# Kernel optimization log

Hardware: AMD Instinct MI355X
Metric: run time of the kernel (lower is better)

Reference implementation:

```python
import jax, jax.numpy as jnp
import numpy as np

N_NODES = 100000
N_EDGES = 100000
NNZ = 3200000
D_IN, D_HID, N_CLS = 512, 16, 7
NEG_SLOPE = 0.2


def _segment_softmax(scores, seg, num_segments, sorted_seg):
    m = jax.ops.segment_max(scores, seg, num_segments=num_segments,
                            indices_are_sorted=sorted_seg)
    ex = jnp.exp(scores - m[seg])
    s = jax.ops.segment_sum(ex, seg, num_segments=num_segments,
                            indices_are_sorted=sorted_seg)
    return ex / (s[seg] + 1e-9)


def _hypergat_layer(X, W, a1, a2, node_idx, edge_idx):
    # X: [N, din] -> h: [N, dout]
    h = X @ W
    hv = h[node_idx]                                   # [nnz, dout] gather
    # phase 1: node -> hyperedge attention (softmax within each hyperedge)
    s1 = jax.nn.leaky_relu(hv @ a1, NEG_SLOPE)         # [nnz]
    alpha = _segment_softmax(s1, edge_idx, N_EDGES, True)
    e = jax.ops.segment_sum(alpha[:, None] * hv, edge_idx,
                            num_segments=N_EDGES, indices_are_sorted=True)
    # phase 2: hyperedge -> node attention (softmax over edges incident to node)
    ev = e[edge_idx]                                   # [nnz, dout] gather
    s2 = jax.nn.leaky_relu(jnp.concatenate([hv, ev], axis=-1) @ a2, NEG_SLOPE)
    beta = _segment_softmax(s2, node_idx, N_NODES, False)
    out = jax.ops.segment_sum(beta[:, None] * ev, node_idx,
                              num_segments=N_NODES)
    return out


def setup_inputs() -> dict:
    key = jax.random.key(0)
    ks = jax.random.split(key, 8)
    H = jax.random.normal(ks[0], (N_NODES, D_IN), dtype=jnp.float32)
    node_idx = jax.random.randint(ks[1], (NNZ,), 0, N_NODES)
    edge_idx = jnp.sort(jax.random.randint(ks[2], (NNZ,), 0, N_EDGES))
    g1 = 1.0 / np.sqrt(D_IN)
    g2 = 1.0 / np.sqrt(D_HID)
    W1 = jax.random.uniform(ks[3], (D_IN, D_HID), jnp.float32, -g1, g1)
    a1_1 = jax.random.uniform(ks[4], (D_HID,), jnp.float32, -g2, g2)
    a2_1 = jax.random.uniform(ks[5], (2 * D_HID,), jnp.float32, -g2, g2)
    W2 = jax.random.uniform(ks[6], (D_HID, N_CLS), jnp.float32, -g2, g2)
    k7, k8 = jax.random.split(ks[7])
    gc = 1.0 / np.sqrt(N_CLS)
    a1_2 = jax.random.uniform(k7, (N_CLS,), jnp.float32, -gc, gc)
    a2_2 = jax.random.uniform(k8, (2 * N_CLS,), jnp.float32, -gc, gc)
    return {"H": H, "W1": W1, "a1_1": a1_1, "a2_1": a2_1,
            "W2": W2, "a1_2": a1_2, "a2_2": a2_2,
            "node_idx": node_idx, "edge_idx": edge_idx}


def reference(H, W1, a1_1, a2_1, W2, a1_2, a2_2, node_idx, edge_idx):
    H1 = _hypergat_layer(H, W1, a1_1, a2_1, node_idx, edge_idx)   # [N, 16]
    X2 = jax.nn.elu(H1)                                           # dropout off (eval)
    H2 = _hypergat_layer(X2, W2, a1_2, a2_2, node_idx, edge_idx)  # [N, 7]
    logp = jax.nn.log_softmax(H2, axis=1)
    return (logp, H1, H2)
```

## Files before the change

kernel.cpp:

```cpp
#include <hip/hip_runtime.h>
#include <hip/hip_bf16.h>
#include <math.h>

#define N_NODES 100000
#define N_EDGESC 100000
#define NNZ_C   3200000
#define D_IN    512
#define D_HID   16
#define N_CLS   7
#define NBK     782

#define G_GEMM 1563
#define G_EOFF 12500
#define G_HIST 250
#define G_BIN  250

typedef short short8 __attribute__((ext_vector_type(8)));
typedef float f32x4  __attribute__((ext_vector_type(4)));

__device__ __forceinline__ unsigned short f2bf_rn(float x) {
  unsigned int u = __float_as_uint(x);
  u += 0x7fff + ((u >> 16) & 1);
  return (unsigned short)(u >> 16);
}
__device__ __forceinline__ float bf2f(unsigned short b) {
  return __uint_as_float(((unsigned int)b) << 16);
}

__device__ __forceinline__ void eoff_body(int b, const int* __restrict__ eidx,
                                          int* __restrict__ eoff) {
  int i = b * 256 + threadIdx.x;
  if (i >= NNZ_C) return;
  int ec = eidx[i];
  int ep = (i == 0) ? -1 : eidx[i - 1];
  for (int e = ep + 1; e <= ec; ++e) eoff[e] = i;
  if (i == NNZ_C - 1) {
    for (int e = ec + 1; e <= N_EDGESC; ++e) eoff[e] = NNZ_C;
  }
}

__device__ __forceinline__ void hist_body(int b, const int* __restrict__ nidx,
                                          int* __restrict__ gcnt) {
  __shared__ int lh[NBK];
  int t = threadIdx.x;
  for (int i = t; i < NBK; i += 256) lh[i] = 0;
  __syncthreads();
  int base = b * 12800;
  for (int it = 0; it < 50; ++it) {
    int i = base + it * 256 + t;
    if (i < NNZ_C) atomicAdd(&lh[nidx[i] >> 7], 1);
  }
  __syncthreads();
  for (int i = t; i < NBK; i += 256) {
    int c = lh[i];
    if (c) atomicAdd(&gcnt[i], c);
  }
}

__device__ __forceinline__ void bin_body(int b, const int* __restrict__ nidx,
                                         const int* __restrict__ eidx,
                                         int* __restrict__ bcur, int* __restrict__ binned) {
  __shared__ int lh[NBK];
  __shared__ int gb[NBK];
  int t = threadIdx.x;
  for (int i = t; i < NBK; i += 256) lh[i] = 0;
  __syncthreads();
  int base = b * 12800;
  for (int it = 0; it < 50; ++it) {
    int i = base + it * 256 + t;
    if (i < NNZ_C) atomicAdd(&lh[nidx[i] >> 7], 1);
  }
  __syncthreads();
  for (int i = t; i < NBK; i += 256) {
    int c = lh[i];
    gb[i] = c ? atomicAdd(&bcur[i], c) : 0;
    lh[i] = 0;
  }
  __syncthreads();
  for (int it = 0; it < 50; ++it) {
    int i = base + it * 256 + t;
    if (i < NNZ_C) {
      int v = nidx[i], e = eidx[i];
      int bk = v >> 7;
      int r = atomicAdd(&lh[bk], 1);
      binned[gb[bk] + r] = e | ((v & 127) << 20);
    }
  }
}

__global__ void bscan_kernel(const int* __restrict__ gcnt, int* __restrict__ boff,
                             int* __restrict__ bcur) {
  __shared__ int lds[1024];
  int t = threadIdx.x;
  int v = (t < NBK) ? gcnt[t] : 0;
  lds[t] = v;
  __syncthreads();
  for (int d = 1; d < 1024; d <<= 1) {
    int u = (t >= d) ? lds[t - d] : 0;
    __syncthreads();
    lds[t] += u;
    __syncthreads();
  }
  if (t < NBK) {
    boff[t + 1] = lds[t];
    bcur[t] = lds[t] - v;
  }
  if (t == 0) boff[0] = 0;
}

__global__ void csr_kernel(const int* __restrict__ binned, const int* __restrict__ boff,
                           int* __restrict__ noff, int* __restrict__ perm_e, int N) {
  __shared__ int lh[128];
  __shared__ int lsc[128];
  __shared__ int lcur[128];
  int b = blockIdx.x;
  int t = threadIdx.x;
  int s = boff[b], e = boff[b + 1];
  if (t < 128) lh[t] = 0;
  __syncthreads();
  for (int i = s + t; i < e; i += 256) {
    atomicAdd(&lh[binned[i] >> 20], 1);
  }
  __syncthreads();
  if (t < 128) lsc[t] = lh[t];
  __syncthreads();
  for (int d = 1; d < 128; d <<= 1) {
    int u = (t < 128 && t >= d) ? lsc[t - d] : 0;
    __syncthreads();
    if (t < 128) lsc[t] += u;
    __syncthreads();
  }
  if (t < 128) {
    int excl = lsc[t] - lh[t];
    lcur[t] = excl;
    int n = b * 128 + t;
    if (n <= N) noff[n] = s + excl;
  }
  __syncthreads();
  for (int i = s + t; i < e; i += 256) {
    int p = binned[i];
    int r = atomicAdd(&lcur[p >> 20], 1);
    perm_e[s + r] = p & 0xFFFFF;
  }
}

__device__ __forceinline__ void gemm1_body(int b,
    const float* __restrict__ X, const float* __restrict__ W,
    const float* __restrict__ a1, const float* __restrict__ a2,
    float* __restrict__ Hout, float2* __restrict__ phv) {
  int wid = b * 4 + (threadIdx.x >> 6);
  if (wid >= 6250) return;
  int lane = threadIdx.x & 63;
  int col  = lane & 15;
  int quad = lane >> 4;

  short8 wh[16], wl[16];
#pragma unroll
  for (int c = 0; c < 16; ++c) {
#pragma unroll
    for (int j = 0; j < 8; ++j) {
      float w = W[(c * 32 + quad * 8 + j) * 16 + col];
      unsigned short h = f2bf_rn(w);
      wh[c][j] = (short)h;
      wl[c][j] = (short)f2bf_rn(w - bf2f(h));
    }
  }

  int rowbase = wid * 16;
  const float4* Xr = (const float4*)(X + (size_t)(rowbase + col) * D_IN) + quad * 2;

  f32x4 acc_hh = {0.f, 0.f, 0.f, 0.f};
  f32x4 acc_hl = {0.f, 0.f, 0.f, 0.f};
  f32x4 acc_lh = {0.f, 0.f, 0.f, 0.f};

  float4 u0 = Xr[0], u1 = Xr[1];
#pragma unroll
  for (int c = 0; c < 16; ++c) {
    float4 n0, n1;
    if (c < 15) { n0 = Xr[(c + 1) * 8]; n1 = Xr[(c + 1) * 8 + 1]; }
    float xs[8] = {u0.x, u0.y, u0.z, u0.w, u1.x, u1.y, u1.z, u1.w};
    short8 ah, al;
#pragma unroll
    for (int j = 0; j < 8; ++j) {
      unsigned short h = f2bf_rn(xs[j]);
      ah[j] = (short)h;
      al[j] = (short)f2bf_rn(xs[j] - bf2f(h));
    }
    acc_hh = __builtin_amdgcn_mfma_f32_16x16x32_bf16(ah, wh[c], acc_hh, 0, 0, 0);
    acc_hl = __builtin_amdgcn_mfma_f32_16x16x32_bf16(ah, wl[c], acc_hl, 0, 0, 0);
    acc_lh = __builtin_amdgcn_mfma_f32_16x16x32_bf16(al, wh[c], acc_lh, 0, 0, 0);
    u0 = n0; u1 = n1;
  }

  float a1c = a1[col], a2c = a2[col];
#pragma unroll
  for (int r = 0; r < 4; ++r) {
    float v = acc_hh[r] + acc_hl[r] + acc_lh[r];
    int row = rowbase + quad * 4 + r;
    Hout[(size_t)row * 16 + col] = v;
    float p1 = v * a1c, p2 = v * a2c;
#pragma unroll
    for (int d = 1; d < 16; d <<= 1) { p1 += __shfl_xor(p1, d); p2 += __shfl_xor(p2, d); }
    if (col == 0) phv[row] = make_float2(p1, p2);
  }
}

__global__ __launch_bounds__(256) void k1_kernel(
    const float* __restrict__ X, const float* __restrict__ W1,
    const float* __restrict__ a1, const float* __restrict__ a2,
    float* __restrict__ Hout, float2* __restrict__ phv,
    const int* __restrict__ eidx, int* __restrict__ eoff,
    const int* __restrict__ nidx, int* __restrict__ gcnt) {
  int b = blockIdx.x;
  if (b < G_GEMM) {
    gemm1_body(b, X, W1, a1, a2, Hout, phv);
  } else if (b < G_GEMM + G_EOFF) {
    eoff_body(b - G_GEMM, eidx, eoff);
  } else {
    hist_body(b - G_GEMM - G_EOFF, nidx, gcnt);
  }
}

template <int D, int GROUP>
__device__ __forceinline__ void edge_body(
    const float* __restrict__ h, const float2* __restrict__ phv,
    const float* __restrict__ a2, const int* __restrict__ eoff,
    const int* __restrict__ nidx, float* __restrict__ eout,
    float* __restrict__ pe, int E, int wave, int lane) {
  constexpr int NG = 64 / GROUP;
  if (wave >= E) return;
  int o0 = eoff[wave], o1 = eoff[wave + 1];
  int g = lane / GROUP, t = lane % GROUP;
  if (o0 == o1) {
    if (g == 0) {
      if (t < D) eout[(size_t)wave * D + t] = 0.f;
      if (t == 0) pe[wave] = 0.f;
    }
    return;
  }
  float m = -1e30f, l = 0.f, acc = 0.f;
  for (int i = o0 + g; i < o1; i += 2 * NG) {
    int i2 = i + NG;
    bool okb = i2 < o1;
    int va = nidx[i];
    int vb = okb ? nidx[i2] : va;
    float pa_ = phv[va].x;
    float pb_ = phv[vb].x;
    float ha = (t < D) ? h[(size_t)va * D + t] : 0.f;
    float hb = (t < D) ? h[(size_t)vb * D + t] : 0.f;
    float sa = pa_ > 0.f ? pa_ : 0.2f * pa_;
    float sb = pb_ > 0.f ? pb_ : 0.2f * pb_;
    if (!okb) sb = -1e30f;
    float mn = fmaxf(m, fmaxf(sa, sb));
    float eo = __expf(m - mn);
    float exa = __expf(sa - mn);
    float exb = __expf(sb - mn);
    l = l * eo + exa + exb;
    acc = acc * eo + exa * ha + exb * hb;
    m = mn;
  }
#pragma unroll
  for (int d = GROUP; d < 64; d <<= 1) {
    float mo = __shfl_xor(m, d), lo = __shfl_xor(l, d), ao = __shfl_xor(acc, d);
    float mn = fmaxf(m, mo);
    float e0 = __expf(m - mn), e1x = __expf(mo - mn);
    l = l * e0 + lo * e1x;
    acc = acc * e0 + ao * e1x;
    m = mn;
  }
  float val = acc / (l + 1e-9f);
  float pav = (t < D) ? val * a2[D + t] : 0.f;
#pragma unroll
  for (int d = 1; d < GROUP; d <<= 1) pav += __shfl_xor(pav, d);
  if (g == 0) {
    if (t < D) eout[(size_t)wave * D + t] = val;
    if (t == 0) pe[wave] = pav;
  }
}

template <int D, int GROUP>
__global__ void edge_kernel(const float* __restrict__ h, const float2* __restrict__ phv,
                            const float* __restrict__ a2, const int* __restrict__ eoff,
                            const int* __restrict__ nidx, float* __restrict__ eout,
                            float* __restrict__ pe, int E) {
  int wave = (blockIdx.x * blockDim.x + threadIdx.x) >> 6;
  edge_body<D, GROUP>(h, phv, a2, eoff, nidx, eout, pe, E, wave, threadIdx.x & 63);
}

__global__ void k3_kernel(const int* __restrict__ nidx, const int* __restrict__ eidx,
                          int* __restrict__ bcur, int* __restrict__ binned,
                          const float* __restrict__ h1g, const float2* __restrict__ phv,
                          const float* __restrict__ a2_1, const int* __restrict__ eoff,
                          float* __restrict__ e1, float* __restrict__ pe) {
  int b = blockIdx.x;
  if (b < G_BIN) {
    bin_body(b, nidx, eidx, bcur, binned);
  } else {
    int wave = (b - G_BIN) * 4 + (threadIdx.x >> 6);
    edge_body<D_HID, 16>(h1g, phv, a2_1, eoff, nidx, e1, pe, N_EDGESC,
                         wave, threadIdx.x & 63);
  }
}

__global__ void node1_kernel(float2* phv, const float* __restrict__ e1,
                             const float* __restrict__ pe, const int* __restrict__ noff,
                             const int* __restrict__ perm_e, float* __restrict__ H1out,
                             float* __restrict__ h2g, const float* __restrict__ W2,
                             const float* __restrict__ a1_2, const float* __restrict__ a2_2,
                             int N) {
  int wave = (blockIdx.x * blockDim.x + threadIdx.x) >> 6;
  int lane = threadIdx.x & 63;
  if (wave >= N) return;
  int o0 = noff[wave], o1 = noff[wave + 1];
  int g = lane >> 4, t = lane & 15;
  float ph = phv[wave].y;
  float m = -1e30f, l = 0.f, acc = 0.f;
  for (int i = o0 + g; i < o1; i += 8) {
    int i2 = i + 4;
    bool okb = i2 < o1;
    int ea = perm_e[i];
    int eb = okb ? perm_e[i2] : ea;
    float pa_ = ph + pe[ea];
    float pb_ = ph + pe[eb];
    float va = e1[(size_t)ea * 16 + t];
    float vb = e1[(size_t)eb * 16 + t];
    float sa = pa_ > 0.f ? pa_ : 0.2f * pa_;
    float sb = pb_ > 0.f ? pb_ : 0.2f * pb_;
    if (!okb) sb = -1e30f;
    float mn = fmaxf(m, fmaxf(sa, sb));
    float eo = __expf(m - mn);
    float exa = __expf(sa - mn);
    float exb = __expf(sb - mn);
    l = l * eo + exa + exb;
    acc = acc * eo + exa * va + exb * vb;
    m = mn;
  }
#pragma unroll
  for (int d = 16; d < 64; d <<= 1) {
    float mo = __shfl_xor(m, d), lo = __shfl_xor(l, d), ao = __shfl_xor(acc, d);
    float mn = fmaxf(m, mo);
    float e0 = __expf(m - mn), e1x = __expf(mo - mn);
    l = l * e0 + lo * e1x;
    acc = acc * e0 + ao * e1x;
    m = mn;
  }
  float val = acc / (l + 1e-9f);
  if (g == 0) H1out[(size_t)wave * 16 + t] = val;
  float x = val > 0.f ? val : expm1f(val);
  float p1 = 0.f, p2 = 0.f, myh2 = 0.f;
#pragma unroll
  for (int j = 0; j < N_CLS; ++j) {
    float term = x * W2[t * N_CLS + j];
#pragma unroll
    for (int d = 1; d < 16; d <<= 1) term += __shfl_xor(term, d);
    p1 += term * a1_2[j];
    p2 += term * a2_2[j];
    if (t == j) myh2 = term;
  }
  if (g == 0) {
    if (t < N_CLS) h2g[(size_t)wave * N_CLS + t] = myh2;
    if (t == 0) phv[wave] = make_float2(p1, p2);
  }
}

__global__ void node2_kernel(const float2* __restrict__ phv, const float* __restrict__ e2,
                             const float* __restrict__ pe, const int* __restrict__ noff,
                             const int* __restrict__ perm_e, float* __restrict__ H2out,
                             float* __restrict__ logp, int N) {
  int wave = (blockIdx.x * blockDim.x + threadIdx.x) >> 6;
  int lane = threadIdx.x & 63;
  if (wave >= N) return;
  int o0 = noff[wave], o1 = noff[wave + 1];
  int g = lane >> 3, t = lane & 7;
  float ph = phv[wave].y;
  float m = -1e30f, l = 0.f, acc = 0.f;
  for (int i = o0 + g; i < o1; i += 16) {
    int i2 = i + 8;
    bool okb = i2 < o1;
    int ea = perm_e[i];
    int eb = okb ? perm_e[i2] : ea;
    float pa_ = ph + pe[ea];
    float pb_ = ph + pe[eb];
    float va = (t < N_CLS) ? e2[(size_t)ea * N_CLS + t] : 0.f;
    float vb = (t < N_CLS) ? e2[(size_t)eb * N_CLS + t] : 0.f;
    float sa = pa_ > 0.f ? pa_ : 0.2f * pa_;
    float sb = pb_ > 0.f ? pb_ : 0.2f * pb_;
    if (!okb) sb = -1e30f;
    float mn = fmaxf(m, fmaxf(sa, sb));
    float eo = __expf(m - mn);
    float exa = __expf(sa - mn);
    float exb = __expf(sb - mn);
    l = l * eo + exa + exb;
    acc = acc * eo + exa * va + exb * vb;
    m = mn;
  }
#pragma unroll
  for (int d = 8; d < 64; d <<= 1) {
    float mo = __shfl_xor(m, d), lo = __shfl_xor(l, d), ao = __shfl_xor(acc, d);
    float mn = fmaxf(m, mo);
    float e0 = __expf(m - mn), e1x = __expf(mo - mn);
    l = l * e0 + lo * e1x;
    acc = acc * e0 + ao * e1x;
    m = mn;
  }
  float val = acc / (l + 1e-9f);
  if (g == 0 && t < N_CLS) H2out[(size_t)wave * N_CLS + t] = val;
  float xm = (t < N_CLS) ? val : -1e30f;
#pragma unroll
  for (int d = 1; d < 8; d <<= 1) xm = fmaxf(xm, __shfl_xor(xm, d));
  float se = (t < N_CLS) ? __expf(val - xm) : 0.f;
#pragma unroll
  for (int d = 1; d < 8; d <<= 1) se += __shfl_xor(se, d);
  float lg = logf(se);
  if (g == 0 && t < N_CLS) logp[(size_t)wave * N_CLS + t] = val - xm - lg;
}

extern "C" void kernel_launch(void* const* d_in, const int* in_sizes, int n_in,
                              void* d_out, int out_size, void* d_ws, size_t ws_size,
                              hipStream_t stream) {
  const float* H    = (const float*)d_in[0];
  const float* W1   = (const float*)d_in[1];
  const float* a1_1 = (const float*)d_in[2];
  const float* a2_1 = (const float*)d_in[3];
  const float* W2   = (const float*)d_in[4];
  const float* a1_2 = (const float*)d_in[5];
  const float* a2_2 = (const float*)d_in[6];
  const int* nidx   = (const int*)d_in[7];
  const int* eidx   = (const int*)d_in[8];

  float* outp = (float*)d_out;
  float* logp = outp;
  float* H1   = outp + (size_t)N_NODES * N_CLS;
  float* H2   = H1 + (size_t)N_NODES * D_HID;

  char* ws = (char*)d_ws;
  float* h1g  = (float*)(ws + 0);
  float* e1   = (float*)(ws + 6400000);
  float* h2g  = (float*)(ws + 12800000);
  float* e2   = (float*)(ws + 15600000);
  int* eoff   = (int*)(ws + 18400000);
  int* noff   = (int*)(ws + 18800128);
  float* pe   = (float*)(ws + 19200256);
  int* perm_e = (int*)(ws + 19600384);
  float2* phv = (float2*)(ws + 32400384);
  int* gcnt   = (int*)(ws + 33200384);
  int* boff   = (int*)(ws + 33203584);
  int* bcur   = (int*)(ws + 33206784);
  int* binned = (int*)(ws + 33210368);

  const int TB = 256;

  hipMemsetAsync(gcnt, 0, NBK * sizeof(int), stream);
  k1_kernel<<<G_GEMM + G_EOFF + G_HIST, TB, 0, stream>>>(
      H, W1, a1_1, a2_1, h1g, phv, eidx, eoff, nidx, gcnt);
  bscan_kernel<<<1, 1024, 0, stream>>>(gcnt, boff, bcur);
  k3_kernel<<<G_BIN + 25000, TB, 0, stream>>>(
      nidx, eidx, bcur, binned, h1g, phv, a2_1, eoff, e1, pe);
  csr_kernel<<<NBK, TB, 0, stream>>>(binned, boff, noff, perm_e, N_NODES);
  node1_kernel<<<25000, TB, 0, stream>>>(phv, e1, pe, noff, perm_e, H1, h2g,
                                         W2, a1_2, a2_2, N_NODES);
  edge_kernel<N_CLS, 8><<<25000, TB, 0, stream>>>(h2g, phv, a2_2, eoff, nidx, e2, pe, N_EDGESC);
  node2_kernel<<<25000, TB, 0, stream>>>(phv, e2, pe, noff, perm_e, H2, logp, N_NODES);
}
```

Before: 660.8 us.

## Cooperatively load segment indices, vectorize eoff, rebalance hist/bin blocks, deepen GEMM prefetch

The gather loops in the edge and node kernels now load up to 64 segment indices coalesced, one per lane, and broadcast them with shuffles instead of each group issuing its own scattered index loads. The eoff builder processes four indices per thread with an int4 load, and the histogram and binning bodies use four times as many blocks, each handling a smaller chunk with no bounds check. The layer-1 GEMM prefetches X two iterations ahead instead of one, and launch bounds are added to several kernels. Together these aim to cut load latency and improve parallelism in the sparse passes, at the cost of extra shuffle instructions and more global atomics into the histogram counters.

```diff
diff --git a/kernel.cpp b/kernel.cpp
--- a/kernel.cpp
+++ b/kernel.cpp
@@ -11,9 +11,9 @@
 #define NBK     782
 
 #define G_GEMM 1563
-#define G_EOFF 12500
-#define G_HIST 250
-#define G_BIN  250
+#define G_HIST 1000
+#define G_EOFF 3125
+#define G_BIN  1000
 
 typedef short short8 __attribute__((ext_vector_type(8)));
 typedef float f32x4  __attribute__((ext_vector_type(4)));
@@ -29,13 +29,18 @@
 
 __device__ __forceinline__ void eoff_body(int b, const int* __restrict__ eidx,
                                           int* __restrict__ eoff) {
-  int i = b * 256 + threadIdx.x;
-  if (i >= NNZ_C) return;
-  int ec = eidx[i];
-  int ep = (i == 0) ? -1 : eidx[i - 1];
-  for (int e = ep + 1; e <= ec; ++e) eoff[e] = i;
-  if (i == NNZ_C - 1) {
-    for (int e = ec + 1; e <= N_EDGESC; ++e) eoff[e] = NNZ_C;
+  int i0 = (b * 256 + threadIdx.x) * 4;
+  if (i0 >= NNZ_C) return;
+  int4 v4 = *(const int4*)(eidx + i0);
+  int vv[4] = {v4.x, v4.y, v4.z, v4.w};
+  int prev = (i0 == 0) ? -1 : eidx[i0 - 1];
+#pragma unroll
+  for (int k = 0; k < 4; ++k) {
+    for (int e = prev + 1; e <= vv[k]; ++e) eoff[e] = i0 + k;
+    prev = vv[k];
+  }
+  if (i0 + 4 == NNZ_C) {
+    for (int e = prev + 1; e <= N_EDGESC; ++e) eoff[e] = NNZ_C;
   }
 }
 
@@ -45,11 +50,8 @@
   int t = threadIdx.x;
   for (int i = t; i < NBK; i += 256) lh[i] = 0;
   __syncthreads();
-  int base = b * 12800;
-  for (int it = 0; it < 50; ++it) {
-    int i = base + it * 256 + t;
-    if (i < NNZ_C) atomicAdd(&lh[nidx[i] >> 7], 1);
-  }
+  int base = b * 3200, end = base + 3200;
+  for (int i = base + t; i < end; i += 256) atomicAdd(&lh[nidx[i] >> 7], 1);
   __syncthreads();
   for (int i = t; i < NBK; i += 256) {
     int c = lh[i];
@@ -65,11 +67,8 @@
   int t = threadIdx.x;
   for (int i = t; i < NBK; i += 256) lh[i] = 0;
   __syncthreads();
-  int base = b * 12800;
-  for (int it = 0; it < 50; ++it) {
-    int i = base + it * 256 + t;
-    if (i < NNZ_C) atomicAdd(&lh[nidx[i] >> 7], 1);
-  }
+  int base = b * 3200, end = base + 3200;
+  for (int i = base + t; i < end; i += 256) atomicAdd(&lh[nidx[i] >> 7], 1);
   __syncthreads();
   for (int i = t; i < NBK; i += 256) {
     int c = lh[i];
@@ -77,14 +76,11 @@
     lh[i] = 0;
   }
   __syncthreads();
-  for (int it = 0; it < 50; ++it) {
-    int i = base + it * 256 + t;
-    if (i < NNZ_C) {
-      int v = nidx[i], e = eidx[i];
-      int bk = v >> 7;
-      int r = atomicAdd(&lh[bk], 1);
-      binned[gb[bk] + r] = e | ((v & 127) << 20);
-    }
+  for (int i = base + t; i < end; i += 256) {
+    int v = nidx[i], e = eidx[i];
+    int bk = v >> 7;
+    int r = atomicAdd(&lh[bk], 1);
+    binned[gb[bk] + r] = e | ((v & 127) << 20);
   }
 }
 
@@ -173,12 +169,13 @@
   f32x4 acc_hl = {0.f, 0.f, 0.f, 0.f};
   f32x4 acc_lh = {0.f, 0.f, 0.f, 0.f};
 
-  float4 u0 = Xr[0], u1 = Xr[1];
+  float4 A0 = Xr[0], A1 = Xr[1];
+  float4 B0 = Xr[8], B1 = Xr[9];
 #pragma unroll
   for (int c = 0; c < 16; ++c) {
-    float4 n0, n1;
-    if (c < 15) { n0 = Xr[(c + 1) * 8]; n1 = Xr[(c + 1) * 8 + 1]; }
-    float xs[8] = {u0.x, u0.y, u0.z, u0.w, u1.x, u1.y, u1.z, u1.w};
+    float4 C0 = B0, C1 = B1;
+    if (c < 14) { C0 = Xr[(c + 2) * 8]; C1 = Xr[(c + 2) * 8 + 1]; }
+    float xs[8] = {A0.x, A0.y, A0.z, A0.w, A1.x, A1.y, A1.z, A1.w};
     short8 ah, al;
 #pragma unroll
     for (int j = 0; j < 8; ++j) {
@@ -189,7 +186,7 @@
     acc_hh = __builtin_amdgcn_mfma_f32_16x16x32_bf16(ah, wh[c], acc_hh, 0, 0, 0);
     acc_hl = __builtin_amdgcn_mfma_f32_16x16x32_bf16(ah, wl[c], acc_hl, 0, 0, 0);
     acc_lh = __builtin_amdgcn_mfma_f32_16x16x32_bf16(al, wh[c], acc_lh, 0, 0, 0);
-    u0 = n0; u1 = n1;
+    A0 = B0; A1 = B1; B0 = C0; B1 = C1;
   }
 
   float a1c = a1[col], a2c = a2[col];
@@ -207,17 +204,17 @@
 
 __global__ __launch_bounds__(256) void k1_kernel(
     const float* __restrict__ X, const float* __restrict__ W1,
-    const float* __restrict__ a1, const float* __restrict__ a2,
+    const float* __restrict__ a1_1, const float* __restrict__ a2_1,
     float* __restrict__ Hout, float2* __restrict__ phv,
     const int* __restrict__ eidx, int* __restrict__ eoff,
     const int* __restrict__ nidx, int* __restrict__ gcnt) {
   int b = blockIdx.x;
   if (b < G_GEMM) {
-    gemm1_body(b, X, W1, a1, a2, Hout, phv);
-  } else if (b < G_GEMM + G_EOFF) {
-    eoff_body(b - G_GEMM, eidx, eoff);
+    gemm1_body(b, X, W1, a1_1, a2_1, Hout, phv);
+  } else if (b < G_GEMM + G_HIST) {
+    hist_body(b - G_GEMM, nidx, gcnt);
   } else {
-    hist_body(b - G_GEMM - G_EOFF, nidx, gcnt);
+    eoff_body(b - G_GEMM - G_HIST, eidx, eoff);
   }
 }
 
@@ -239,25 +236,30 @@
     return;
   }
   float m = -1e30f, l = 0.f, acc = 0.f;
-  for (int i = o0 + g; i < o1; i += 2 * NG) {
-    int i2 = i + NG;
-    bool okb = i2 < o1;
-    int va = nidx[i];
-    int vb = okb ? nidx[i2] : va;
-    float pa_ = phv[va].x;
-    float pb_ = phv[vb].x;
-    float ha = (t < D) ? h[(size_t)va * D + t] : 0.f;
-    float hb = (t < D) ? h[(size_t)vb * D + t] : 0.f;
-    float sa = pa_ > 0.f ? pa_ : 0.2f * pa_;
-    float sb = pb_ > 0.f ? pb_ : 0.2f * pb_;
-    if (!okb) sb = -1e30f;
-    float mn = fmaxf(m, fmaxf(sa, sb));
-    float eo = __expf(m - mn);
-    float exa = __expf(sa - mn);
-    float exb = __expf(sb - mn);
-    l = l * eo + exa + exb;
-    acc = acc * eo + exa * ha + exb * hb;
-    m = mn;
+  for (int base = o0; base < o1; base += 64) {
+    int nrem = o1 - base; if (nrem > 64) nrem = 64;
+    int li = base + lane;
+    int idx_l = nidx[li < o1 ? li : o1 - 1];
+    for (int jb = 0; jb < nrem; jb += 2 * NG) {
+      int j = jb + g;
+      bool oka = j < nrem;
+      bool okb = j + NG < nrem;
+      int va = __shfl(idx_l, j);
+      int vb = __shfl(idx_l, j + NG);
+      float pa_ = phv[va].x;
+      float pb_ = phv[vb].x;
+      float ha = (t < D) ? h[(size_t)va * D + t] : 0.f;
+      float hb = (t < D) ? h[(size_t)vb * D + t] : 0.f;
+      float sa = oka ? (pa_ > 0.f ? pa_ : 0.2f * pa_) : -1e30f;
+      float sb = okb ? (pb_ > 0.f ? pb_ : 0.2f * pb_) : -1e30f;
+      float mn = fmaxf(m, fmaxf(sa, sb));
+      float eo = __expf(m - mn);
+      float exa = oka ? __expf(sa - mn) : 0.f;
+      float exb = okb ? __expf(sb - mn) : 0.f;
+      l = l * eo + exa + exb;
+      acc = acc * eo + exa * ha + exb * hb;
+      m = mn;
+    }
   }
 #pragma unroll
   for (int d = GROUP; d < 64; d <<= 1) {
@@ -279,19 +281,21 @@
 }
 
 template <int D, int GROUP>
-__global__ void edge_kernel(const float* __restrict__ h, const float2* __restrict__ phv,
-                            const float* __restrict__ a2, const int* __restrict__ eoff,
-                            const int* __restrict__ nidx, float* __restrict__ eout,
-                            float* __restrict__ pe, int E) {
+__global__ __launch_bounds__(256) void edge_kernel(
+    const float* __restrict__ h, const float2* __restrict__ phv,
+    const float* __restrict__ a2, const int* __restrict__ eoff,
+    const int* __restrict__ nidx, float* __restrict__ eout,
+    float* __restrict__ pe, int E) {
   int wave = (blockIdx.x * blockDim.x + threadIdx.x) >> 6;
   edge_body<D, GROUP>(h, phv, a2, eoff, nidx, eout, pe, E, wave, threadIdx.x & 63);
 }
 
-__global__ void k3_kernel(const int* __restrict__ nidx, const int* __restrict__ eidx,
-                          int* __restrict__ bcur, int* __restrict__ binned,
-                          const float* __restrict__ h1g, const float2* __restrict__ phv,
-                          const float* __restrict__ a2_1, const int* __restrict__ eoff,
-                          float* __restrict__ e1, float* __restrict__ pe) {
+__global__ __launch_bounds__(256) void k3_kernel(
+    const int* __restrict__ nidx, const int* __restrict__ eidx,
+    int* __restrict__ bcur, int* __restrict__ binned,
+    const float* __restrict__ h1g, const float2* __restrict__ phv,
+    const float* __restrict__ a2_1, const int* __restrict__ eoff,
+    float* __restrict__ e1, float* __restrict__ pe) {
   int b = blockIdx.x;
   if (b < G_BIN) {
     bin_body(b, nidx, eidx, bcur, binned);
@@ -302,46 +306,51 @@
   }
 }
 
-__global__ void node1_kernel(float2* phv, const float* __restrict__ e1,
-                             const float* __restrict__ pe, const int* __restrict__ noff,
-                             const int* __restrict__ perm_e, float* __restrict__ H1out,
-                             float* __restrict__ h2g, const float* __restrict__ W2,
-                             const float* __restrict__ a1_2, const float* __restrict__ a2_2,
-                             int N) {
+__global__ __launch_bounds__(256) void node1_kernel(
+    float2* phv, const float* __restrict__ e1,
+    const float* __restrict__ pe, const int* __restrict__ noff,
+    const int* __restrict__ perm_e, float* __restrict__ H1out,
+    float* __restrict__ h2g, const float* __restrict__ W2,
+    const float* __restrict__ a1_2, const float* __restrict__ a2_2) {
   int wave = (blockIdx.x * blockDim.x + threadIdx.x) >> 6;
   int lane = threadIdx.x & 63;
-  if (wave >= N) return;
+  if (wave >= N_NODES) return;
   int o0 = noff[wave], o1 = noff[wave + 1];
   int g = lane >> 4, t = lane & 15;
   float ph = phv[wave].y;
   float m = -1e30f, l = 0.f, acc = 0.f;
-  for (int i = o0 + g; i < o1; i += 8) {
-    int i2 = i + 4;
-    bool okb = i2 < o1;
-    int ea = perm_e[i];
-    int eb = okb ? perm_e[i2] : ea;
-    float pa_ = ph + pe[ea];
-    float pb_ = ph + pe[eb];
-    float va = e1[(size_t)ea * 16 + t];
-    float vb = e1[(size_t)eb * 16 + t];
-    float sa = pa_ > 0.f ? pa_ : 0.2f * pa_;
-    float sb = pb_ > 0.f ? pb_ : 0.2f * pb_;
-    if (!okb) sb = -1e30f;
-    float mn = fmaxf(m, fmaxf(sa, sb));
-    float eo = __expf(m - mn);
-    float exa = __expf(sa - mn);
-    float exb = __expf(sb - mn);
-    l = l * eo + exa + exb;
-    acc = acc * eo + exa * va + exb * vb;
-    m = mn;
+  for (int base = o0; base < o1; base += 64) {
+    int nrem = o1 - base; if (nrem > 64) nrem = 64;
+    int li = base + lane;
+    int idx_l = perm_e[li < o1 ? li : o1 - 1];
+    for (int jb = 0; jb < nrem; jb += 8) {
+      int j = jb + g;
+      bool oka = j < nrem;
+      bool okb = j + 4 < nrem;
+      int ea = __shfl(idx_l, j);
+      int eb = __shfl(idx_l, j + 4);
+      float pa_ = ph + pe[ea];
+      float pb_ = ph + pe[eb];
+      float va = e1[(size_t)ea * 16 + t];
+      float vb = e1[(size_t)eb * 16 + t];
+      float sa = oka ? (pa_ > 0.f ? pa_ : 0.2f * pa_) : -1e30f;
+      float sb = okb ? (pb_ > 0.f ? pb_ : 0.2f * pb_) : -1e30f;
+      float mn = fmaxf(m, fmaxf(sa, sb));
+      float eo = __expf(m - mn);
+      float exa = oka ? __expf(sa - mn) : 0.f;
+      float exb = okb ? __expf(sb - mn) : 0.f;
+      l = l * eo + exa + exb;
+      acc = acc * eo + exa * va + exb * vb;
+      m = mn;
+    }
   }
 #pragma unroll
   for (int d = 16; d < 64; d <<= 1) {
     float mo = __shfl_xor(m, d), lo = __shfl_xor(l, d), ao = __shfl_xor(acc, d);
     float mn = fmaxf(m, mo);
-    float e0 = __expf(m - mn), e1x = __expf(mo - mn);
-    l = l * e0 + lo * e1x;
-    acc = acc * e0 + ao * e1x;
+    float ea = __expf(m - mn), eb = __expf(mo - mn);
+    l = l * ea + lo * eb;
+    acc = acc * ea + ao * eb;
     m = mn;
   }
   float val = acc / (l + 1e-9f);
@@ -363,44 +372,50 @@
   }
 }
 
-__global__ void node2_kernel(const float2* __restrict__ phv, const float* __restrict__ e2,
-                             const float* __restrict__ pe, const int* __restrict__ noff,
-                             const int* __restrict__ perm_e, float* __restrict__ H2out,
-                             float* __restrict__ logp, int N) {
+__global__ __launch_bounds__(256) void node2_kernel(
+    const float2* __restrict__ phv, const float* __restrict__ e2,
+    const float* __restrict__ pe, const int* __restrict__ noff,
+    const int* __restrict__ perm_e, float* __restrict__ H2out,
+    float* __restrict__ logp) {
   int wave = (blockIdx.x * blockDim.x + threadIdx.x) >> 6;
   int lane = threadIdx.x & 63;
-  if (wave >= N) return;
+  if (wave >= N_NODES) return;
   int o0 = noff[wave], o1 = noff[wave + 1];
   int g = lane >> 3, t = lane & 7;
   float ph = phv[wave].y;
   float m = -1e30f, l = 0.f, acc = 0.f;
-  for (int i = o0 + g; i < o1; i += 16) {
-    int i2 = i + 8;
-    bool okb = i2 < o1;
-    int ea = perm_e[i];
-    int eb = okb ? perm_e[i2] : ea;
-    float pa_ = ph + pe[ea];
-    float pb_ = ph + pe[eb];
-    float va = (t < N_CLS) ? e2[(size_t)ea * N_CLS + t] : 0.f;
-    float vb = (t < N_CLS) ? e2[(size_t)eb * N_CLS + t] : 0.f;
-    float sa = pa_ > 0.f ? pa_ : 0.2f * pa_;
-    float sb = pb_ > 0.f ? pb_ : 0.2f * pb_;
-    if (!okb) sb = -1e30f;
-    float mn = fmaxf(m, fmaxf(sa, sb));
-    float eo = __expf(m - mn);
-    float exa = __expf(sa - mn);
-    float exb = __expf(sb - mn);
-    l = l * eo + exa + exb;
-    acc = acc * eo + exa * va + exb * vb;
-    m = mn;
+  for (int base = o0; base < o1; base += 64) {
+    int nrem = o1 - base; if (nrem > 64) nrem = 64;
+    int li = base + lane;
+    int idx_l = perm_e[li < o1 ? li : o1 - 1];
+    for (int jb = 0; jb < nrem; jb += 16) {
+      int j = jb + g;
+      bool oka = j < nrem;
+      bool okb = j + 8 < nrem;
+      int ea = __shfl(idx_l, j);
+      int eb = __shfl(idx_l, j + 8);
+      float pa_ = ph + pe[ea];
+      float pb_ = ph + pe[eb];
+      float va = (t < N_CLS) ? e2[(size_t)ea * N_CLS + t] : 0.f;
+      float vb = (t < N_CLS) ? e2[(size_t)eb * N_CLS + t] : 0.f;
+      float sa = oka ? (pa_ > 0.f ? pa_ : 0.2f * pa_) : -1e30f;
+      float sb = okb ? (pb_ > 0.f ? pb_ : 0.2f * pb_) : -1e30f;
+      float mn = fmaxf(m, fmaxf(sa, sb));
+      float eo = __expf(m - mn);
+      float exa = oka ? __expf(sa - mn) : 0.f;
+      float exb = okb ? __expf(sb - mn) : 0.f;
+      l = l * eo + exa + exb;
+      acc = acc * eo + exa * va + exb * vb;
+      m = mn;
+    }
   }
 #pragma unroll
   for (int d = 8; d < 64; d <<= 1) {
     float mo = __shfl_xor(m, d), lo = __shfl_xor(l, d), ao = __shfl_xor(acc, d);
     float mn = fmaxf(m, mo);
-    float e0 = __expf(m - mn), e1x = __expf(mo - mn);
-    l = l * e0 + lo * e1x;
-    acc = acc * e0 + ao * e1x;
+    float ea = __expf(m - mn), eb = __expf(mo - mn);
+    l = l * ea + lo * eb;
+    acc = acc * ea + ao * eb;
     m = mn;
   }
   float val = acc / (l + 1e-9f);
@@ -451,14 +466,14 @@
   const int TB = 256;
 
   hipMemsetAsync(gcnt, 0, NBK * sizeof(int), stream);
-  k1_kernel<<<G_GEMM + G_EOFF + G_HIST, TB, 0, stream>>>(
+  k1_kernel<<<G_GEMM + G_HIST + G_EOFF, TB, 0, stream>>>(
       H, W1, a1_1, a2_1, h1g, phv, eidx, eoff, nidx, gcnt);
   bscan_kernel<<<1, 1024, 0, stream>>>(gcnt, boff, bcur);
   k3_kernel<<<G_BIN + 25000, TB, 0, stream>>>(
       nidx, eidx, bcur, binned, h1g, phv, a2_1, eoff, e1, pe);
   csr_kernel<<<NBK, TB, 0, stream>>>(binned, boff, noff, perm_e, N_NODES);
   node1_kernel<<<25000, TB, 0, stream>>>(phv, e1, pe, noff, perm_e, H1, h2g,
-                                         W2, a1_2, a2_2, N_NODES);
+                                         W2, a1_2, a2_2);
   edge_kernel<N_CLS, 8><<<25000, TB, 0, stream>>>(h2g, phv, a2_2, eoff, nidx, e2, pe, N_EDGESC);
-  node2_kernel<<<25000, TB, 0, stream>>>(phv, e2, pe, noff, perm_e, H2, logp, N_NODES);
-}
+  node2_kernel<<<25000, TB, 0, stream>>>(phv, e2, pe, noff, perm_e, H2, logp);
+}
```

New measurement: 627.1 us. 5.1% less time.
